# Kernel optimization log

Measured on AMD Instinct MI355X. Metric: run time of the kernel, lower is better.

## Reference

```python
import jax, jax.numpy as jnp
import numpy as np

B, S, N, H, C = 64, 512, 24, 768, 6

CONST_LAST = jnp.array([0.1, 0.1, 0.1, 0.3, 0.8, 0.01], dtype=jnp.float32)
CONST_MID = jnp.array([0.1, 0.1, 0.1, 0.8, 0.3, 0.01], dtype=jnp.float32)


def setup_inputs() -> dict:
    key = jax.random.key(0)
    k1, k2, k3, k4 = jax.random.split(key, 4)
    last_hidden_state = jax.random.normal(k1, (B, S, H), dtype=jnp.float32)
    # strictly increasing boundaries in [0, S-1]: sort randint in [0, S-N) then add arange(N)
    base = jnp.sort(jax.random.randint(k2, (B, N), 0, S - N), axis=1)
    sentence_token = base + jnp.arange(N, dtype=base.dtype)[None, :]
    W = jax.random.normal(k3, (C, H), dtype=jnp.float32) * 0.02
    b = jax.random.normal(k4, (C,), dtype=jnp.float32) * 0.02
    return {"last_hidden_state": last_hidden_state, "sentence_token": sentence_token,
            "W": W, "b": b}


def reference(last_hidden_state, sentence_token, W, b):
    # last_hidden_state: [B,S,H]; sentence_token: [B,N] strictly increasing boundaries.
    # Segment j covers tokens [prev+1, t_j] inclusive (prev = -1 for j==0).
    ends = sentence_token                                            # [B,N]
    prev = jnp.concatenate([-jnp.ones_like(ends[:, :1]), ends[:, :-1]], axis=1)
    # prefix sums with leading zero: csp[:, t+1] = sum of tokens 0..t
    cs = jnp.cumsum(last_hidden_state, axis=1)                       # [B,S,H]
    csp = jnp.concatenate([jnp.zeros_like(cs[:, :1]), cs], axis=1)   # [B,S+1,H]
    seg_sum = (jnp.take_along_axis(csp, (ends + 1)[:, :, None], axis=1)
               - jnp.take_along_axis(csp, (prev + 1)[:, :, None], axis=1))  # [B,N,H]
    lens = (ends - prev).astype(last_hidden_state.dtype)[:, :, None]  # >= 1 by construction
    seg_mean = seg_sum / lens                                         # [B,N,H]
    probs = jax.nn.sigmoid(jnp.einsum('bnh,ch->bnc', seg_mean, W) + b)  # [B,N,C]
    # override: boundary > 500 -> constant probability vector (different if last sentence)
    is_last = (jnp.arange(ends.shape[1]) == ends.shape[1] - 1)[None, :, None]  # [1,N,1]
    const = jnp.where(is_last, CONST_LAST[None, None, :], CONST_MID[None, None, :])
    over = (ends > 500)[:, :, None]
    return jnp.where(over, const, probs)
```

## Files before the change

### kernel.cpp

```cpp
#include <hip/hip_runtime.h>
#include <math.h>

#define B_ 64
#define S_ 512
#define N_ 24
#define H_ 768
#define C_ 6
#define CHUNKS 16
#define TOK_PER_BLOCK (S_ / CHUNKS)
#define TOK_PER_WAVE (TOK_PER_BLOCK / 4)

__global__ __launch_bounds__(256, 2) void seg_proj_kernel(
    const float* __restrict__ lhs, const int* __restrict__ st,
    const float* __restrict__ W, float* __restrict__ outbuf, int use_atomic) {
  __shared__ float acc[N_ * C_ * 64];
  const int tid = threadIdx.x;
  const int lane = tid & 63;
  const int wave = tid >> 6;
  const int b = blockIdx.x / CHUNKS;
  const int chunk = blockIdx.x % CHUNKS;

  float4* accv = (float4*)acc;
#pragma unroll
  for (int i = 0; i < 9; ++i)
    accv[i * 256 + tid] = make_float4(0.f, 0.f, 0.f, 0.f);

  int stb_l = (lane < N_) ? st[b * N_ + lane] : 0x7fffffff;

  const float4* W4 = (const float4*)W;
  float4 w[3][C_];
#pragma unroll
  for (int k = 0; k < 3; ++k)
#pragma unroll
    for (int c = 0; c < C_; ++c)
      w[k][c] = W4[c * (H_ / 4) + k * 64 + lane];
#pragma unroll
  for (int k = 0; k < 3; ++k)
    asm volatile("" : "+v"(w[k][0].x), "+v"(w[k][0].y), "+v"(w[k][0].z), "+v"(w[k][0].w),
                       "+v"(w[k][1].x), "+v"(w[k][1].y), "+v"(w[k][1].z), "+v"(w[k][1].w),
                       "+v"(w[k][2].x), "+v"(w[k][2].y), "+v"(w[k][2].z), "+v"(w[k][2].w),
                       "+v"(w[k][3].x), "+v"(w[k][3].y), "+v"(w[k][3].z), "+v"(w[k][3].w),
                       "+v"(w[k][4].x), "+v"(w[k][4].y), "+v"(w[k][4].z), "+v"(w[k][4].w),
                       "+v"(w[k][5].x), "+v"(w[k][5].y), "+v"(w[k][5].z), "+v"(w[k][5].w));

  __syncthreads();

  const int s_base = chunk * TOK_PER_BLOCK + wave * TOK_PER_WAVE;
  const float4* x4 = (const float4*)(lhs + ((size_t)b * S_ + s_base) * H_);
  float4 x[TOK_PER_WAVE][3];
#pragma unroll
  for (int t = 0; t < TOK_PER_WAVE; ++t) {
    x[t][0] = x4[t * 192 + lane];
    x[t][1] = x4[t * 192 + 64 + lane];
    x[t][2] = x4[t * 192 + 128 + lane];
  }

  float racc[C_] = {0.f, 0.f, 0.f, 0.f, 0.f, 0.f};
  int cur_seg = N_;
#pragma unroll
  for (int t = 0; t < TOK_PER_WAVE; ++t) {
    const int s = s_base + t;
    const int seg = (int)__popcll(__ballot(stb_l < s));
    if (seg != cur_seg) {
      if (cur_seg < N_) {
#pragma unroll
        for (int c = 0; c < C_; ++c)
          atomicAdd(&acc[(cur_seg * C_ + c) * 64 + lane], racc[c]);
      }
#pragma unroll
      for (int c = 0; c < C_; ++c) racc[c] = 0.f;
      cur_seg = seg;
    }
#pragma unroll
    for (int k = 0; k < 3; ++k)
#pragma unroll
      for (int c = 0; c < C_; ++c)
        racc[c] += x[t][k].x * w[k][c].x + x[t][k].y * w[k][c].y +
                   x[t][k].z * w[k][c].z + x[t][k].w * w[k][c].w;
  }
  if (cur_seg < N_) {
#pragma unroll
    for (int c = 0; c < C_; ++c)
      atomicAdd(&acc[(cur_seg * C_ + c) * 64 + lane], racc[c]);
  }

  __syncthreads();
  if (tid < N_ * C_) {
    float v = 0.f;
    const int base = tid * 64;
#pragma unroll 8
    for (int i = 0; i < 64; ++i) v += acc[base + ((i + tid) & 63)];
    if (use_atomic)
      atomicAdd(&outbuf[b * N_ * C_ + tid], v);
    else
      outbuf[(size_t)blockIdx.x * (N_ * C_) + tid] = v;
  }
}

__global__ __launch_bounds__(256) void finalize_kernel(
    const float* __restrict__ buf, const int* __restrict__ st,
    const float* __restrict__ bias, float* __restrict__ out, int use_atomic) {
  int idx = blockIdx.x * blockDim.x + threadIdx.x;
  if (idx >= B_ * N_ * C_) return;
  int c = idx % C_;
  int j = (idx / C_) % N_;
  int b = idx / (N_ * C_);
  float ssum;
  if (use_atomic) {
    ssum = buf[idx];
  } else {
    ssum = 0.f;
#pragma unroll
    for (int k = 0; k < CHUNKS; ++k)
      ssum += buf[(size_t)(b * CHUNKS + k) * (N_ * C_) + j * C_ + c];
  }
  int end = st[b * N_ + j];
  int prev = (j == 0) ? -1 : st[b * N_ + j - 1];
  float len = (float)(end - prev);
  float logit = ssum / len + bias[c];
  float p = 1.0f / (1.0f + expf(-logit));
  if (end > 500) {
    float cl = (c < 3) ? 0.1f : (c == 3 ? 0.3f : (c == 4 ? 0.8f : 0.01f));
    float cm = (c < 3) ? 0.1f : (c == 3 ? 0.8f : (c == 4 ? 0.3f : 0.01f));
    p = (j == N_ - 1) ? cl : cm;
  }
  out[idx] = p;
}

extern "C" void kernel_launch(void* const* d_in, const int* in_sizes, int n_in,
                              void* d_out, int out_size, void* d_ws, size_t ws_size,
                              hipStream_t stream) {
  const float* lhs  = (const float*)d_in[0];
  const int*   st   = (const int*)d_in[1];
  const float* W    = (const float*)d_in[2];
  const float* bias = (const float*)d_in[3];

  const size_t need = (size_t)B_ * CHUNKS * N_ * C_ * sizeof(float);
  const int use_atomic = (ws_size < need) ? 1 : 0;
  if (use_atomic)
    hipMemsetAsync(d_ws, 0, (size_t)B_ * N_ * C_ * sizeof(float), stream);

  seg_proj_kernel<<<B_ * CHUNKS, 256, 0, stream>>>(lhs, st, W, (float*)d_ws, use_atomic);
  finalize_kernel<<<(B_ * N_ * C_ + 255) / 256, 256, 0, stream>>>(
      (float*)d_ws, st, bias, (float*)d_out, use_atomic);
}
```

Measured before the change: 153.9 us.

## Fuse projection and finalize into one cooperative kernel with grid sync

```diff
diff --git a/kernel.cpp b/kernel.cpp
--- a/kernel.cpp
+++ b/kernel.cpp
@@ -1,14 +1,139 @@
 #include <hip/hip_runtime.h>
+#include <hip/hip_cooperative_groups.h>
 #include <math.h>
+
+namespace cg = cooperative_groups;
 
 #define B_ 64
 #define S_ 512
 #define N_ 24
 #define H_ 768
 #define C_ 6
-#define CHUNKS 16
-#define TOK_PER_BLOCK (S_ / CHUNKS)
-#define TOK_PER_WAVE (TOK_PER_BLOCK / 4)
+#define OUT_ELEMS (B_ * N_ * C_)
+
+#define FCH 8
+#define FTOK (S_ / FCH)
+#define FTOKW (FTOK / 4)
+#define FGRID (B_ * FCH)
+
+__global__ __launch_bounds__(256, 2) void fused_kernel(
+    const float* __restrict__ lhs, const int* __restrict__ st,
+    const float* __restrict__ W, const float* __restrict__ bias,
+    float* __restrict__ out) {
+  __shared__ float acc[N_ * C_ * 64];
+  const int tid = threadIdx.x;
+  const int lane = tid & 63;
+  const int wave = tid >> 6;
+  const int b = blockIdx.x >> 3;
+  const int chunk = blockIdx.x & 7;
+  const int flat = blockIdx.x * 256 + tid;
+
+  if (flat < OUT_ELEMS) atomicExch(&out[flat], 0.0f);
+
+  float4* accv = (float4*)acc;
+#pragma unroll
+  for (int i = 0; i < 9; ++i)
+    accv[i * 256 + tid] = make_float4(0.f, 0.f, 0.f, 0.f);
+
+  int stb_l = (lane < N_) ? st[b * N_ + lane] : 0x7fffffff;
+
+  const float4* W4 = (const float4*)W;
+  float4 w[3][C_];
+#pragma unroll
+  for (int k = 0; k < 3; ++k)
+#pragma unroll
+    for (int c = 0; c < C_; ++c)
+      w[k][c] = W4[c * (H_ / 4) + k * 64 + lane];
+#pragma unroll
+  for (int k = 0; k < 3; ++k)
+    asm volatile("" : "+v"(w[k][0].x), "+v"(w[k][0].y), "+v"(w[k][0].z), "+v"(w[k][0].w),
+                       "+v"(w[k][1].x), "+v"(w[k][1].y), "+v"(w[k][1].z), "+v"(w[k][1].w),
+                       "+v"(w[k][2].x), "+v"(w[k][2].y), "+v"(w[k][2].z), "+v"(w[k][2].w),
+                       "+v"(w[k][3].x), "+v"(w[k][3].y), "+v"(w[k][3].z), "+v"(w[k][3].w),
+                       "+v"(w[k][4].x), "+v"(w[k][4].y), "+v"(w[k][4].z), "+v"(w[k][4].w),
+                       "+v"(w[k][5].x), "+v"(w[k][5].y), "+v"(w[k][5].z), "+v"(w[k][5].w));
+
+  __syncthreads();
+
+  const int s_base = chunk * FTOK + wave * FTOKW;
+  const float4* x4 = (const float4*)(lhs + ((size_t)b * S_ + s_base) * H_);
+
+  float racc[C_] = {0.f, 0.f, 0.f, 0.f, 0.f, 0.f};
+  int cur_seg = N_;
+#pragma unroll 1
+  for (int h = 0; h < 2; ++h) {
+    float4 x[8][3];
+#pragma unroll
+    for (int t = 0; t < 8; ++t) {
+      const int tt = h * 8 + t;
+      x[t][0] = x4[tt * 192 + lane];
+      x[t][1] = x4[tt * 192 + 64 + lane];
+      x[t][2] = x4[tt * 192 + 128 + lane];
+    }
+#pragma unroll
+    for (int t = 0; t < 8; ++t) {
+      const int s = s_base + h * 8 + t;
+      const int seg = (int)__popcll(__ballot(stb_l < s));
+      if (seg != cur_seg) {
+        if (cur_seg < N_) {
+#pragma unroll
+          for (int c = 0; c < C_; ++c)
+            atomicAdd(&acc[(cur_seg * C_ + c) * 64 + lane], racc[c]);
+        }
+#pragma unroll
+        for (int c = 0; c < C_; ++c) racc[c] = 0.f;
+        cur_seg = seg;
+      }
+#pragma unroll
+      for (int k = 0; k < 3; ++k)
+#pragma unroll
+        for (int c = 0; c < C_; ++c)
+          racc[c] += x[t][k].x * w[k][c].x + x[t][k].y * w[k][c].y +
+                     x[t][k].z * w[k][c].z + x[t][k].w * w[k][c].w;
+    }
+  }
+  if (cur_seg < N_) {
+#pragma unroll
+    for (int c = 0; c < C_; ++c)
+      atomicAdd(&acc[(cur_seg * C_ + c) * 64 + lane], racc[c]);
+  }
+
+  __syncthreads();
+
+  float v = 0.f;
+  if (tid < N_ * C_) {
+    const int base = tid * 64;
+#pragma unroll 8
+    for (int i = 0; i < 64; ++i) v += acc[base + ((i + tid) & 63)];
+  }
+
+  cg::this_grid().sync();
+
+  if (tid < N_ * C_) atomicAdd(&out[b * N_ * C_ + tid], v);
+
+  cg::this_grid().sync();
+
+  if (flat < OUT_ELEMS) {
+    const float ssum = atomicAdd(&out[flat], 0.0f);
+    const int c = flat % C_;
+    const int j = (flat / C_) % N_;
+    const int bb = flat / (N_ * C_);
+    const int end = st[bb * N_ + j];
+    const int prev = (j == 0) ? -1 : st[bb * N_ + j - 1];
+    const float logit = ssum / (float)(end - prev) + bias[c];
+    float p = 1.0f / (1.0f + expf(-logit));
+    if (end > 500) {
+      const float cl = (c < 3) ? 0.1f : (c == 3 ? 0.3f : (c == 4 ? 0.8f : 0.01f));
+      const float cm = (c < 3) ? 0.1f : (c == 3 ? 0.8f : (c == 4 ? 0.3f : 0.01f));
+      p = (j == N_ - 1) ? cl : cm;
+    }
+    out[flat] = p;
+  }
+}
+
+#define OCH 16
+#define OTB (S_ / OCH)
+#define OTW (OTB / 4)
 
 __global__ __launch_bounds__(256, 2) void seg_proj_kernel(
     const float* __restrict__ lhs, const int* __restrict__ st,
@@ -17,8 +142,8 @@
   const int tid = threadIdx.x;
   const int lane = tid & 63;
   const int wave = tid >> 6;
-  const int b = blockIdx.x / CHUNKS;
-  const int chunk = blockIdx.x % CHUNKS;
+  const int b = blockIdx.x / OCH;
+  const int chunk = blockIdx.x % OCH;
 
   float4* accv = (float4*)acc;
 #pragma unroll
@@ -45,11 +170,11 @@
 
   __syncthreads();
 
-  const int s_base = chunk * TOK_PER_BLOCK + wave * TOK_PER_WAVE;
+  const int s_base = chunk * OTB + wave * OTW;
   const float4* x4 = (const float4*)(lhs + ((size_t)b * S_ + s_base) * H_);
-  float4 x[TOK_PER_WAVE][3];
-#pragma unroll
-  for (int t = 0; t < TOK_PER_WAVE; ++t) {
+  float4 x[OTW][3];
+#pragma unroll
+  for (int t = 0; t < OTW; ++t) {
     x[t][0] = x4[t * 192 + lane];
     x[t][1] = x4[t * 192 + 64 + lane];
     x[t][2] = x4[t * 192 + 128 + lane];
@@ -58,7 +183,7 @@
   float racc[C_] = {0.f, 0.f, 0.f, 0.f, 0.f, 0.f};
   int cur_seg = N_;
 #pragma unroll
-  for (int t = 0; t < TOK_PER_WAVE; ++t) {
+  for (int t = 0; t < OTW; ++t) {
     const int s = s_base + t;
     const int seg = (int)__popcll(__ballot(stb_l < s));
     if (seg != cur_seg) {
@@ -111,8 +236,8 @@
   } else {
     ssum = 0.f;
 #pragma unroll
-    for (int k = 0; k < CHUNKS; ++k)
-      ssum += buf[(size_t)(b * CHUNKS + k) * (N_ * C_) + j * C_ + c];
+    for (int k = 0; k < OCH; ++k)
+      ssum += buf[(size_t)(b * OCH + k) * (N_ * C_) + j * C_ + c];
   }
   int end = st[b * N_ + j];
   int prev = (j == 0) ? -1 : st[b * N_ + j - 1];
@@ -134,13 +259,18 @@
   const int*   st   = (const int*)d_in[1];
   const float* W    = (const float*)d_in[2];
   const float* bias = (const float*)d_in[3];
-
-  const size_t need = (size_t)B_ * CHUNKS * N_ * C_ * sizeof(float);
-  const int use_atomic = (ws_size < need) ? 1 : 0;
-  if (use_atomic)
-    hipMemsetAsync(d_ws, 0, (size_t)B_ * N_ * C_ * sizeof(float), stream);
-
-  seg_proj_kernel<<<B_ * CHUNKS, 256, 0, stream>>>(lhs, st, W, (float*)d_ws, use_atomic);
-  finalize_kernel<<<(B_ * N_ * C_ + 255) / 256, 256, 0, stream>>>(
-      (float*)d_ws, st, bias, (float*)d_out, use_atomic);
-}
+  float* out = (float*)d_out;
+
+  void* args[] = {(void*)&lhs, (void*)&st, (void*)&W, (void*)&bias, (void*)&out};
+  hipError_t e = hipLaunchCooperativeKernel((const void*)fused_kernel, dim3(FGRID),
+                                            dim3(256), (void**)args, 0, stream);
+  if (e != hipSuccess) {
+    const size_t need = (size_t)B_ * OCH * N_ * C_ * sizeof(float);
+    const int use_atomic = (ws_size < need) ? 1 : 0;
+    if (use_atomic)
+      hipMemsetAsync(d_ws, 0, (size_t)B_ * N_ * C_ * sizeof(float), stream);
+    seg_proj_kernel<<<B_ * OCH, 256, 0, stream>>>(lhs, st, W, (float*)d_ws, use_atomic);
+    finalize_kernel<<<(B_ * N_ * C_ + 255) / 256, 256, 0, stream>>>(
+        (float*)d_ws, st, bias, out, use_atomic);
+  }
+}
```

Result: slower. 267.1 us (+73.5%).

## Assign one block per segment and fuse projection, mean and sigmoid into one kernel

Applied to the files above, without the earlier changes.

```diff
diff --git a/kernel.cpp b/kernel.cpp
--- a/kernel.cpp
+++ b/kernel.cpp
@@ -6,26 +6,32 @@
 #define N_ 24
 #define H_ 768
 #define C_ 6
-#define CHUNKS 16
-#define TOK_PER_BLOCK (S_ / CHUNKS)
-#define TOK_PER_WAVE (TOK_PER_BLOCK / 4)
 
-__global__ __launch_bounds__(256, 2) void seg_proj_kernel(
+__global__ __launch_bounds__(256, 4) void seg_kernel(
     const float* __restrict__ lhs, const int* __restrict__ st,
-    const float* __restrict__ W, float* __restrict__ outbuf, int use_atomic) {
-  __shared__ float acc[N_ * C_ * 64];
+    const float* __restrict__ W, const float* __restrict__ bias,
+    float* __restrict__ out) {
+  const int j = blockIdx.x;
+  const int b = blockIdx.y;
   const int tid = threadIdx.x;
   const int lane = tid & 63;
   const int wave = tid >> 6;
-  const int b = blockIdx.x / CHUNKS;
-  const int chunk = blockIdx.x % CHUNKS;
 
-  float4* accv = (float4*)acc;
-#pragma unroll
-  for (int i = 0; i < 9; ++i)
-    accv[i * 256 + tid] = make_float4(0.f, 0.f, 0.f, 0.f);
+  const int end = st[b * N_ + j];
+  const int prev = (j == 0) ? -1 : st[b * N_ + j - 1];
+  float* o = out + ((size_t)b * N_ + j) * C_;
 
-  int stb_l = (lane < N_) ? st[b * N_ + lane] : 0x7fffffff;
+  if (end > 500) {
+    if (tid < C_) {
+      const int c = tid;
+      const float cl = (c < 3) ? 0.1f : (c == 3 ? 0.3f : (c == 4 ? 0.8f : 0.01f));
+      const float cm = (c < 3) ? 0.1f : (c == 3 ? 0.8f : (c == 4 ? 0.3f : 0.01f));
+      o[c] = (j == N_ - 1) ? cl : cm;
+    }
+    return;
+  }
+
+  __shared__ float sacc[4][C_];
 
   const float4* W4 = (const float4*)W;
   float4 w[3][C_];
@@ -43,88 +49,60 @@
                        "+v"(w[k][4].x), "+v"(w[k][4].y), "+v"(w[k][4].z), "+v"(w[k][4].w),
                        "+v"(w[k][5].x), "+v"(w[k][5].y), "+v"(w[k][5].z), "+v"(w[k][5].w));
 
+  const int start = prev + 1;
+  const int len = end - start + 1;
+  const int nr = (len - wave + 3) >> 2;
+
+  const float4* x4 = (const float4*)(lhs + ((size_t)b * S_ + start + wave) * H_);
+
+  float racc[C_] = {0.f, 0.f, 0.f, 0.f, 0.f, 0.f};
+#pragma unroll 1
+  for (int r0 = 0; r0 < nr; r0 += 8) {
+    float4 x[8][3];
+#pragma unroll
+    for (int t = 0; t < 8; ++t) {
+      if (r0 + t < nr) {
+        const int off = (r0 + t) * 768;
+        x[t][0] = x4[off + lane];
+        x[t][1] = x4[off + 64 + lane];
+        x[t][2] = x4[off + 128 + lane];
+      }
+    }
+#pragma unroll
+    for (int t = 0; t < 8; ++t) {
+      if (r0 + t < nr) {
+#pragma unroll
+        for (int k = 0; k < 3; ++k)
+#pragma unroll
+          for (int c = 0; c < C_; ++c)
+            racc[c] += x[t][k].x * w[k][c].x + x[t][k].y * w[k][c].y +
+                       x[t][k].z * w[k][c].z + x[t][k].w * w[k][c].w;
+      }
+    }
+  }
+
+#pragma unroll
+  for (int c = 0; c < C_; ++c) {
+    float v = racc[c];
+    v += __shfl_xor(v, 1);
+    v += __shfl_xor(v, 2);
+    v += __shfl_xor(v, 4);
+    v += __shfl_xor(v, 8);
+    v += __shfl_xor(v, 16);
+    v += __shfl_xor(v, 32);
+    racc[c] = v;
+  }
+  if (lane == 0) {
+#pragma unroll
+    for (int c = 0; c < C_; ++c) sacc[wave][c] = racc[c];
+  }
   __syncthreads();
 
-  const int s_base = chunk * TOK_PER_BLOCK + wave * TOK_PER_WAVE;
-  const float4* x4 = (const float4*)(lhs + ((size_t)b * S_ + s_base) * H_);
-  float4 x[TOK_PER_WAVE][3];
-#pragma unroll
-  for (int t = 0; t < TOK_PER_WAVE; ++t) {
-    x[t][0] = x4[t * 192 + lane];
-    x[t][1] = x4[t * 192 + 64 + lane];
-    x[t][2] = x4[t * 192 + 128 + lane];
+  if (tid < C_) {
+    const float ssum = sacc[0][tid] + sacc[1][tid] + sacc[2][tid] + sacc[3][tid];
+    const float logit = ssum / (float)len + bias[tid];
+    o[tid] = 1.0f / (1.0f + expf(-logit));
   }
-
-  float racc[C_] = {0.f, 0.f, 0.f, 0.f, 0.f, 0.f};
-  int cur_seg = N_;
-#pragma unroll
-  for (int t = 0; t < TOK_PER_WAVE; ++t) {
-    const int s = s_base + t;
-    const int seg = (int)__popcll(__ballot(stb_l < s));
-    if (seg != cur_seg) {
-      if (cur_seg < N_) {
-#pragma unroll
-        for (int c = 0; c < C_; ++c)
-          atomicAdd(&acc[(cur_seg * C_ + c) * 64 + lane], racc[c]);
-      }
-#pragma unroll
-      for (int c = 0; c < C_; ++c) racc[c] = 0.f;
-      cur_seg = seg;
-    }
-#pragma unroll
-    for (int k = 0; k < 3; ++k)
-#pragma unroll
-      for (int c = 0; c < C_; ++c)
-        racc[c] += x[t][k].x * w[k][c].x + x[t][k].y * w[k][c].y +
-                   x[t][k].z * w[k][c].z + x[t][k].w * w[k][c].w;
-  }
-  if (cur_seg < N_) {
-#pragma unroll
-    for (int c = 0; c < C_; ++c)
-      atomicAdd(&acc[(cur_seg * C_ + c) * 64 + lane], racc[c]);
-  }
-
-  __syncthreads();
-  if (tid < N_ * C_) {
-    float v = 0.f;
-    const int base = tid * 64;
-#pragma unroll 8
-    for (int i = 0; i < 64; ++i) v += acc[base + ((i + tid) & 63)];
-    if (use_atomic)
-      atomicAdd(&outbuf[b * N_ * C_ + tid], v);
-    else
-      outbuf[(size_t)blockIdx.x * (N_ * C_) + tid] = v;
-  }
-}
-
-__global__ __launch_bounds__(256) void finalize_kernel(
-    const float* __restrict__ buf, const int* __restrict__ st,
-    const float* __restrict__ bias, float* __restrict__ out, int use_atomic) {
-  int idx = blockIdx.x * blockDim.x + threadIdx.x;
-  if (idx >= B_ * N_ * C_) return;
-  int c = idx % C_;
-  int j = (idx / C_) % N_;
-  int b = idx / (N_ * C_);
-  float ssum;
-  if (use_atomic) {
-    ssum = buf[idx];
-  } else {
-    ssum = 0.f;
-#pragma unroll
-    for (int k = 0; k < CHUNKS; ++k)
-      ssum += buf[(size_t)(b * CHUNKS + k) * (N_ * C_) + j * C_ + c];
-  }
-  int end = st[b * N_ + j];
-  int prev = (j == 0) ? -1 : st[b * N_ + j - 1];
-  float len = (float)(end - prev);
-  float logit = ssum / len + bias[c];
-  float p = 1.0f / (1.0f + expf(-logit));
-  if (end > 500) {
-    float cl = (c < 3) ? 0.1f : (c == 3 ? 0.3f : (c == 4 ? 0.8f : 0.01f));
-    float cm = (c < 3) ? 0.1f : (c == 3 ? 0.8f : (c == 4 ? 0.3f : 0.01f));
-    p = (j == N_ - 1) ? cl : cm;
-  }
-  out[idx] = p;
 }
 
 extern "C" void kernel_launch(void* const* d_in, const int* in_sizes, int n_in,
@@ -135,12 +113,5 @@
   const float* W    = (const float*)d_in[2];
   const float* bias = (const float*)d_in[3];
 
-  const size_t need = (size_t)B_ * CHUNKS * N_ * C_ * sizeof(float);
-  const int use_atomic = (ws_size < need) ? 1 : 0;
-  if (use_atomic)
-    hipMemsetAsync(d_ws, 0, (size_t)B_ * N_ * C_ * sizeof(float), stream);
-
-  seg_proj_kernel<<<B_ * CHUNKS, 256, 0, stream>>>(lhs, st, W, (float*)d_ws, use_atomic);
-  finalize_kernel<<<(B_ * N_ * C_ + 255) / 256, 256, 0, stream>>>(
-      (float*)d_ws, st, bias, (float*)d_out, use_atomic);
+  seg_kernel<<<dim3(N_, B_), 256, 0, stream>>>(lhs, st, W, bias, (float*)d_out);
 }
```

New measurement: 371.9 us. 2.42x slower.
